# Optimization experiments

Hardware: AMD Instinct MI355X
Metric: run time of the kernel (lower is better)

Reference implementation:

```python
import jax, jax.numpy as jnp
import numpy as np

B, N, HID, E, H = 4, 256, 256, 64, 4
OUT = HID // 2          # 128
D = OUT // H            # 32
AGG = H * (2 * D + 1)   # 260 = concat(mean D, attn_sum 1, max D) per head


def setup_inputs() -> dict:
    key = jax.random.key(0)
    ks = jax.random.split(key, 7)
    s = 0.05
    return {
        "h_x": jax.random.normal(ks[0], (B, N, HID), jnp.float32),
        "h_e": jax.random.normal(ks[1], (B, N, N, E), jnp.float32),
        "h_m": jnp.ones((B, N), jnp.float32),
        "W_Q": jax.random.normal(ks[2], (OUT, HID), jnp.float32) * s,
        "W_K": jax.random.normal(ks[3], (OUT, E), jnp.float32) * s,
        "W_V": jax.random.normal(ks[4], (OUT, E), jnp.float32) * s,
        "W_R": jax.random.normal(ks[5], (OUT, AGG), jnp.float32) * s,
    }


def reference(h_x, h_e, h_m, W_Q, W_K, W_V, W_R):
    # queries from node features: [B,H,N,D]
    h_q = (h_x @ W_Q.T).reshape(B, N, H, D).transpose(0, 2, 1, 3)
    # keys/values from dense pairwise edge features: [B,H,N,N,D]
    h_k = jnp.einsum('bnme,ce->bnmc', h_e, W_K).reshape(B, N, N, H, D).transpose(0, 3, 1, 2, 4)
    h_v = jnp.einsum('bnme,ce->bnmc', h_e, W_V).reshape(B, N, N, H, D).transpose(0, 3, 1, 2, 4)
    # broadcast dot: [B,H,N,N]
    scores = jnp.einsum('bhnd,bhnmd->bhnm', h_q, h_k) / np.float32(np.sqrt(D))
    # per-node mask broadcast as [B,1,N,1] (masks query rows)
    scores = jnp.where(h_m[:, None, :, None] == 0, -jnp.inf, scores)
    # NOTE: original code softmaxes over dim=1 = HEAD axis (faithful)
    attn = jax.nn.softmax(scores, axis=1)                      # [B,H,N,N]
    attn_w = attn[..., None] * h_v                             # [B,H,N,N,D]
    aggr_sum = attn_w.sum(axis=3)                              # [B,H,N,D]
    attn_sum = attn.sum(axis=3, keepdims=True) + 1e-8          # [B,H,N,1]
    aggr_mean = aggr_sum / attn_sum
    aggr_max = attn_w.max(axis=3)                              # [B,H,N,D]
    multi = jnp.concatenate([aggr_mean, attn_sum, aggr_max], axis=-1)  # [B,H,N,2D+1]
    aggr_out = multi.transpose(0, 2, 1, 3).reshape(B, N, AGG)  # [B,N,260]
    return aggr_out @ W_R.T                                    # [B,N,OUT]
```

## Files before the change

kernel.cpp:

```cpp
#include <hip/hip_runtime.h>
#include <hip/hip_bf16.h>

constexpr int Bb   = 4;
constexpr int Nn   = 256;
constexpr int HID  = 256;
constexpr int Ee   = 64;
constexpr int Hh   = 4;
constexpr int OUTc = 128;
constexpr int Dd   = 32;
constexpr int AGG  = 260;
constexpr int REC  = 264;
constexpr int QA_LD = 264;

constexpr size_t WS_WRT   = 0;
constexpr size_t WS_FRAGV = WS_WRT + (size_t)AGG * OUTc;
constexpr size_t WS_FRAGQ = WS_FRAGV + 4096;
constexpr size_t WS_UFRAG = WS_FRAGQ + 16384;

typedef __attribute__((ext_vector_type(8))) short short8;
typedef __attribute__((ext_vector_type(4))) float floatx4;

__device__ __forceinline__ unsigned pk2(float a, float b) {
    union { __hip_bfloat162 h; unsigned u; } cv;
    cv.h = __float22bfloat162_rn(float2{a, b});
    return cv.u;
}

__device__ __forceinline__ short8 pack8(floatx4 f0, floatx4 f1) {
    union { short8 s; unsigned u[4]; } r;
    r.u[0] = pk2(f0[0], f0[1]);
    r.u[1] = pk2(f0[2], f0[3]);
    r.u[2] = pk2(f1[0], f1[1]);
    r.u[3] = pk2(f1[2], f1[3]);
    return r.s;
}

__device__ __forceinline__ void gload16(const float* g, float* l) {
    __builtin_amdgcn_global_load_lds(
        (const __attribute__((address_space(1))) void*)g,
        (__attribute__((address_space(3))) void*)l, 16, 0, 0);
}

__global__ __launch_bounds__(256)
void eama_prep(const float* __restrict__ W_Q, const float* __restrict__ W_V,
               const float* __restrict__ W_R, const float* __restrict__ h_x,
               const float* __restrict__ W_K,
               unsigned short* __restrict__ wfragV, float* __restrict__ W_RT,
               unsigned short* __restrict__ ufrag)
{
    __shared__ __align__(16) unsigned short sA[16 * QA_LD];
    __shared__ __align__(16) float sqL[16][132];
    __shared__ __align__(16) float sU2[16][256];

    const int tid = threadIdx.x;
    const int bid = blockIdx.x;

    if (bid < 4) {
        const int e    = bid * 256 + tid;
        const int lane = e & 63;
        const int ks   = (e >> 6) & 1;
        const int ct   = e >> 7;
        const int ncol = lane & 15, q8 = lane >> 4;
        const float* row = W_V + (ct * 16 + ncol) * Ee;
        const int k0 = ks * 32 + q8 * 8;
        floatx4 f0 = *(const floatx4*)(row + k0);
        floatx4 f1 = *(const floatx4*)(row + k0 + 4);
        *(short8*)(wfragV + (size_t)e * 8) = pack8(f0, f1);
        return;
    }
    if (bid < 134) {
        const int i = (bid - 4) * 256 + tid;
        if (i < AGG * OUTc) {
            const int c = i & 127, j = i >> 7;
            W_RT[j * OUTc + c] = W_R[c * AGG + j];
        }
        return;
    }

    const int b0   = (bid - 134) * 16;
    const int lane = tid & 63;
    const int wv   = tid >> 6;
    const int ncol = lane & 15, q8 = lane >> 4;

    short8 bq[2][8];
    #pragma unroll
    for (int ct = 0; ct < 2; ++ct)
        #pragma unroll
        for (int ks = 0; ks < 8; ++ks) {
            const float* row = W_Q + (size_t)(wv * 32 + ct * 16 + ncol) * HID + ks * 32 + q8 * 8;
            bq[ct][ks] = pack8(*(const floatx4*)row, *(const floatx4*)(row + 4));
        }
    #pragma unroll
    for (int i = 0; i < 2; ++i) {
        const int idx = tid + i * 256;
        const int r = idx >> 5, blk = idx & 31;
        const float* src = h_x + (size_t)(b0 + r) * HID + blk * 8;
        floatx4 f0 = *(const floatx4*)(src);
        floatx4 f1 = *(const floatx4*)(src + 4);
        *(short8*)&sA[r * QA_LD + blk * 8] = pack8(f0, f1);
    }
    __syncthreads();
    floatx4 acc[2] = {(floatx4){0,0,0,0}, (floatx4){0,0,0,0}};
    #pragma unroll
    for (int ks = 0; ks < 8; ++ks) {
        short8 a = *(const short8*)&sA[ncol * QA_LD + ks * 32 + q8 * 8];
        acc[0] = __builtin_amdgcn_mfma_f32_16x16x32_bf16(a, bq[0][ks], acc[0], 0, 0, 0);
        acc[1] = __builtin_amdgcn_mfma_f32_16x16x32_bf16(a, bq[1][ks], acc[1], 0, 0, 0);
    }
    #pragma unroll
    for (int ct = 0; ct < 2; ++ct)
        #pragma unroll
        for (int rr = 0; rr < 4; ++rr)
            sqL[q8 * 4 + rr][wv * 32 + ct * 16 + ncol] = acc[ct][rr];
    __syncthreads();

    {
        const int h = wv, e = lane;
        float a16[16];
        #pragma unroll
        for (int i = 0; i < 16; ++i) a16[i] = 0.f;
        #pragma unroll
        for (int d4 = 0; d4 < 8; ++d4) {
            float wk0 = W_K[(h * Dd + d4 * 4 + 0) * Ee + e];
            float wk1 = W_K[(h * Dd + d4 * 4 + 1) * Ee + e];
            float wk2 = W_K[(h * Dd + d4 * 4 + 2) * Ee + e];
            float wk3 = W_K[(h * Dd + d4 * 4 + 3) * Ee + e];
            #pragma unroll
            for (int b16 = 0; b16 < 16; ++b16) {
                floatx4 qv = *(const floatx4*)&sqL[b16][h * Dd + d4 * 4];
                a16[b16] += (qv[0] * wk0 + qv[1] * wk1) + (qv[2] * wk2 + qv[3] * wk3);
            }
        }
        #pragma unroll
        for (int b16 = 0; b16 < 16; ++b16)
            sU2[b16][h * 64 + e] = a16[b16] * (0.1767766952966369f * 1.4426950408889634f);
    }
    __syncthreads();

    #pragma unroll
    for (int k = 0; k < 8; ++k) {
        const int ei   = tid + k * 256;
        const int b16  = ei >> 7;
        const int rest = ei & 127;
        const int ks   = rest >> 6;
        const int l    = rest & 63;
        const int nc   = l & 15, qq = l >> 4;
        short8 v = {0, 0, 0, 0, 0, 0, 0, 0};
        if (nc < Hh) {
            floatx4 f0 = *(const floatx4*)&sU2[b16][nc * 64 + ks * 32 + qq * 8];
            floatx4 f1 = *(const floatx4*)&sU2[b16][nc * 64 + ks * 32 + qq * 8 + 4];
            v = pack8(f0, f1);
        }
        *(short8*)(ufrag + ((size_t)((b0 + b16) * 2 + ks) * 64 + l) * 8) = v;
    }
}

__global__ __launch_bounds__(256, 2)
void eama_full(const float* __restrict__ h_e, const float* __restrict__ h_m,
               const unsigned short* __restrict__ wfragV,
               const unsigned short* __restrict__ ufrag,
               const float* __restrict__ W_RT, float* __restrict__ out)
{
    __shared__ __align__(16) float sStage[4][2][4][64][4];
    __shared__ __align__(16) float sS[4][16][4];
    __shared__ float sVS[4][OUTc];
    __shared__ float sVM[4][OUTc];
    __shared__ float sAS[4][Hh];
    __shared__ float sAsum[Hh];

    float* sM = &sStage[0][0][0][0][0];
    float (*sAcc)[OUTc] = (float (*)[OUTc])(sM + 384);

    const int tid  = threadIdx.x;
    const int lane = tid & 63;
    const int w    = tid >> 6;
    const int ncol = lane & 15;
    const int q8   = lane >> 4;
    const int bn   = blockIdx.x;
    const float maskv = h_m[bn];

    short8 bfV[8][2];
    #pragma unroll
    for (int ct = 0; ct < 8; ++ct)
        #pragma unroll
        for (int ks = 0; ks < 2; ++ks)
            bfV[ct][ks] = *(const short8*)(wfragV + ((size_t)(ct * 2 + ks) * 64 + lane) * 8);
    short8 bu0 = *(const short8*)(ufrag + ((size_t)(bn * 2 + 0) * 64 + lane) * 8);
    short8 bu1 = *(const short8*)(ufrag + ((size_t)(bn * 2 + 1) * 64 + lane) * 8);
    asm volatile("" ::: "memory");

    const float* heb = h_e + (size_t)bn * Nn * Ee;
    const float* arq = heb + (size_t)(w * 64 + ncol) * Ee + q8 * 8;

    #define STAGE(it_, buf_) do { \
        const float* ar_ = arq + (size_t)(it_) * 16 * Ee; \
        gload16(ar_,      &sStage[w][buf_][0][0][0]); \
        gload16(ar_ + 4,  &sStage[w][buf_][1][0][0]); \
        gload16(ar_ + 32, &sStage[w][buf_][2][0][0]); \
        gload16(ar_ + 36, &sStage[w][buf_][3][0][0]); \
    } while (0)

    STAGE(0, 0);
    STAGE(1, 1);

    float vs[8], vm[8], asumH = 0.f;
    #pragma unroll
    for (int ct = 0; ct < 8; ++ct) { vs[ct] = 0.f; vm[ct] = -3.402823466e38f; }

    #pragma unroll
    for (int it = 0; it < 4; ++it) {
        const int buf = it & 1;
        if (it < 3) asm volatile("s_waitcnt vmcnt(4)" ::: "memory");
        else        asm volatile("s_waitcnt vmcnt(0)" ::: "memory");

        floatx4 c0 = *(const floatx4*)&sStage[w][buf][0][lane][0];
        floatx4 c1 = *(const floatx4*)&sStage[w][buf][1][lane][0];
        floatx4 c2 = *(const floatx4*)&sStage[w][buf][2][lane][0];
        floatx4 c3 = *(const floatx4*)&sStage[w][buf][3][lane][0];
        short8 af0 = pack8(c0, c1);
        short8 af1 = pack8(c2, c3);
        if (it < 2) {
            asm volatile("s_waitcnt lgkmcnt(0)" ::: "memory");
            STAGE(it + 2, buf);
        }

        floatx4 accV[8], accS = (floatx4){0, 0, 0, 0};
        #pragma unroll
        for (int ct = 0; ct < 8; ++ct) accV[ct] = (floatx4){0, 0, 0, 0};
        __builtin_amdgcn_s_setprio(1);
        #pragma unroll
        for (int ct = 0; ct < 8; ++ct) {
            accV[ct] = __builtin_amdgcn_mfma_f32_16x16x32_bf16(af0, bfV[ct][0], accV[ct], 0, 0, 0);
            accV[ct] = __builtin_amdgcn_mfma_f32_16x16x32_bf16(af1, bfV[ct][1], accV[ct], 0, 0, 0);
        }
        accS = __builtin_amdgcn_mfma_f32_16x16x32_bf16(af0, bu0, accS, 0, 0, 0);
        accS = __builtin_amdgcn_mfma_f32_16x16x32_bf16(af1, bu1, accS, 0, 0, 0);
        __builtin_amdgcn_s_setprio(0);

        if (ncol < Hh) {
            #pragma unroll
            for (int r = 0; r < 4; ++r)
                sS[w][q8 * 4 + r][ncol] = (maskv != 0.f) ? accS[r] : -1e30f;
        }
        __builtin_amdgcn_wave_barrier();

        #pragma unroll
        for (int r = 0; r < 4; ++r) {
            floatx4 sc = *(const floatx4*)&sS[w][q8 * 4 + r][0];
            float e0 = __builtin_amdgcn_exp2f(sc[0]), e1 = __builtin_amdgcn_exp2f(sc[1]);
            float e2 = __builtin_amdgcn_exp2f(sc[2]), e3 = __builtin_amdgcn_exp2f(sc[3]);
            float inv = __builtin_amdgcn_rcpf((e0 + e1) + (e2 + e3));
            float a0 = e0 * inv, a1 = e1 * inv, a2 = e2 * inv, a3 = e3 * inv;
            asumH += (ncol & 2) ? ((ncol & 1) ? a3 : a2) : ((ncol & 1) ? a1 : a0);
            float p;
            p = a0 * accV[0][r]; vs[0] += p; vm[0] = fmaxf(vm[0], p);
            p = a0 * accV[1][r]; vs[1] += p; vm[1] = fmaxf(vm[1], p);
            p = a1 * accV[2][r]; vs[2] += p; vm[2] = fmaxf(vm[2], p);
            p = a1 * accV[3][r]; vs[3] += p; vm[3] = fmaxf(vm[3], p);
            p = a2 * accV[4][r]; vs[4] += p; vm[4] = fmaxf(vm[4], p);
            p = a2 * accV[5][r]; vs[5] += p; vm[5] = fmaxf(vm[5], p);
            p = a3 * accV[6][r]; vs[6] += p; vm[6] = fmaxf(vm[6], p);
            p = a3 * accV[7][r]; vs[7] += p; vm[7] = fmaxf(vm[7], p);
        }
        __builtin_amdgcn_wave_barrier();
    }
    #undef STAGE

    #pragma unroll
    for (int ct = 0; ct < 8; ++ct) {
        vs[ct] += __shfl_xor(vs[ct], 16, 64);
        vs[ct] += __shfl_xor(vs[ct], 32, 64);
        vm[ct] = fmaxf(vm[ct], __shfl_xor(vm[ct], 16, 64));
        vm[ct] = fmaxf(vm[ct], __shfl_xor(vm[ct], 32, 64));
    }
    asumH += __shfl_xor(asumH, 16, 64);
    asumH += __shfl_xor(asumH, 32, 64);

    if (lane < 16) {
        #pragma unroll
        for (int ct = 0; ct < 8; ++ct) {
            sVS[w][ct * 16 + lane] = vs[ct];
            sVM[w][ct * 16 + lane] = vm[ct];
        }
    }
    if (lane < Hh) sAS[w][lane] = asumH;
    __syncthreads();
    if (tid < Hh) {
        sAsum[tid] = 1e-8f +
            (sAS[0][tid] + sAS[1][tid]) + (sAS[2][tid] + sAS[3][tid]);
    }
    __syncthreads();
    if (tid < OUTc) {
        float vsum = (sVS[0][tid] + sVS[1][tid]) + (sVS[2][tid] + sVS[3][tid]);
        float vmax = fmaxf(fmaxf(sVM[0][tid], sVM[1][tid]), fmaxf(sVM[2][tid], sVM[3][tid]));
        const int h = tid >> 5, d = tid & 31;
        sM[h * 65 + d]      = vsum / sAsum[h];
        sM[h * 65 + 33 + d] = vmax;
        if (tid < Hh) sM[tid * 65 + 32] = sAsum[tid];
    }
    __syncthreads();
    {
        const int c = tid & 127, part = tid >> 7;
        const int j0 = part * 130;
        float a0 = 0.f, a1 = 0.f, a2 = 0.f, a3 = 0.f;
        #pragma unroll 4
        for (int j = j0; j < j0 + 128; j += 4) {
            a0 = fmaf(sM[j],     W_RT[(j)     * OUTc + c], a0);
            a1 = fmaf(sM[j + 1], W_RT[(j + 1) * OUTc + c], a1);
            a2 = fmaf(sM[j + 2], W_RT[(j + 2) * OUTc + c], a2);
            a3 = fmaf(sM[j + 3], W_RT[(j + 3) * OUTc + c], a3);
        }
        a0 = fmaf(sM[j0 + 128], W_RT[(j0 + 128) * OUTc + c], a0);
        a1 = fmaf(sM[j0 + 129], W_RT[(j0 + 129) * OUTc + c], a1);
        sAcc[part][c] = (a0 + a1) + (a2 + a3);
    }
    __syncthreads();
    if (tid < OUTc)
        out[bn * OUTc + tid] = sAcc[0][tid] + sAcc[1][tid];
}

extern "C" void kernel_launch(void* const* d_in, const int* in_sizes, int n_in,
                              void* d_out, int out_size, void* d_ws, size_t ws_size,
                              hipStream_t stream) {
    const float* h_x = (const float*)d_in[0];
    const float* h_e = (const float*)d_in[1];
    const float* h_m = (const float*)d_in[2];
    const float* W_Q = (const float*)d_in[3];
    const float* W_K = (const float*)d_in[4];
    const float* W_V = (const float*)d_in[5];
    const float* W_R = (const float*)d_in[6];
    float* out = (float*)d_out;

    float* ws            = (float*)d_ws;
    float* W_RT          = ws + WS_WRT;
    unsigned short* wfV  = (unsigned short*)(ws + WS_FRAGV);
    unsigned short* ufr  = (unsigned short*)(ws + WS_UFRAG);

    eama_prep<<<dim3(198), dim3(256), 0, stream>>>(W_Q, W_V, W_R, h_x, W_K, wfV, W_RT, ufr);
    eama_full<<<dim3(Bb * Nn), dim3(256), 0, stream>>>(h_e, h_m, wfV, ufr, W_RT, out);
}
```

Baseline: 125.8 us.

## Move V weight fragments to LDS and prefetch edge tiles into registers

The per-wave register copy of the W_V bf16 fragments is replaced by a block-wide LDS copy that is read each iteration before the MFMAs. The global_load_lds double-buffered staging of h_e is replaced by a register prefetch of the next 16-row tile. Launch bounds go from 2 to 4 blocks per CU. The aim is to cut VGPR pressure and raise occupancy so more waves hide the h_e streaming latency, at the cost of extra LDS reads per MFMA and an added block barrier.

```diff
diff --git a/kernel.cpp b/kernel.cpp
--- a/kernel.cpp
+++ b/kernel.cpp
@@ -33,12 +33,6 @@
     r.u[2] = pk2(f1[0], f1[1]);
     r.u[3] = pk2(f1[2], f1[3]);
     return r.s;
-}
-
-__device__ __forceinline__ void gload16(const float* g, float* l) {
-    __builtin_amdgcn_global_load_lds(
-        (const __attribute__((address_space(1))) void*)g,
-        (__attribute__((address_space(3))) void*)l, 16, 0, 0);
 }
 
 __global__ __launch_bounds__(256)
@@ -155,21 +149,20 @@
     }
 }
 
-__global__ __launch_bounds__(256, 2)
+__global__ __launch_bounds__(256, 4)
 void eama_full(const float* __restrict__ h_e, const float* __restrict__ h_m,
                const unsigned short* __restrict__ wfragV,
                const unsigned short* __restrict__ ufrag,
                const float* __restrict__ W_RT, float* __restrict__ out)
 {
-    __shared__ __align__(16) float sStage[4][2][4][64][4];
+    __shared__ __align__(16) unsigned short sBF[1024 * 8];
     __shared__ __align__(16) float sS[4][16][4];
     __shared__ float sVS[4][OUTc];
     __shared__ float sVM[4][OUTc];
     __shared__ float sAS[4][Hh];
     __shared__ float sAsum[Hh];
-
-    float* sM = &sStage[0][0][0][0][0];
-    float (*sAcc)[OUTc] = (float (*)[OUTc])(sM + 384);
+    __shared__ __align__(16) float sM[REC];
+    __shared__ float sAcc[2][OUTc];
 
     const int tid  = threadIdx.x;
     const int lane = tid & 63;
@@ -179,50 +172,40 @@
     const int bn   = blockIdx.x;
     const float maskv = h_m[bn];
 
-    short8 bfV[8][2];
-    #pragma unroll
-    for (int ct = 0; ct < 8; ++ct)
-        #pragma unroll
-        for (int ks = 0; ks < 2; ++ks)
-            bfV[ct][ks] = *(const short8*)(wfragV + ((size_t)(ct * 2 + ks) * 64 + lane) * 8);
+    #pragma unroll
+    for (int i = 0; i < 4; ++i) {
+        const int e = i * 256 + tid;
+        *(floatx4*)&sBF[(size_t)e * 8] = *(const floatx4*)(wfragV + (size_t)e * 8);
+    }
     short8 bu0 = *(const short8*)(ufrag + ((size_t)(bn * 2 + 0) * 64 + lane) * 8);
     short8 bu1 = *(const short8*)(ufrag + ((size_t)(bn * 2 + 1) * 64 + lane) * 8);
-    asm volatile("" ::: "memory");
+    __syncthreads();
 
     const float* heb = h_e + (size_t)bn * Nn * Ee;
     const float* arq = heb + (size_t)(w * 64 + ncol) * Ee + q8 * 8;
 
-    #define STAGE(it_, buf_) do { \
-        const float* ar_ = arq + (size_t)(it_) * 16 * Ee; \
-        gload16(ar_,      &sStage[w][buf_][0][0][0]); \
-        gload16(ar_ + 4,  &sStage[w][buf_][1][0][0]); \
-        gload16(ar_ + 32, &sStage[w][buf_][2][0][0]); \
-        gload16(ar_ + 36, &sStage[w][buf_][3][0][0]); \
-    } while (0)
-
-    STAGE(0, 0);
-    STAGE(1, 1);
-
     float vs[8], vm[8], asumH = 0.f;
     #pragma unroll
     for (int ct = 0; ct < 8; ++ct) { vs[ct] = 0.f; vm[ct] = -3.402823466e38f; }
 
+    floatx4 p0, p1, p2, p3;
+    p0 = *(const floatx4*)(arq);
+    p1 = *(const floatx4*)(arq + 4);
+    p2 = *(const floatx4*)(arq + 32);
+    p3 = *(const floatx4*)(arq + 36);
+
     #pragma unroll
     for (int it = 0; it < 4; ++it) {
-        const int buf = it & 1;
-        if (it < 3) asm volatile("s_waitcnt vmcnt(4)" ::: "memory");
-        else        asm volatile("s_waitcnt vmcnt(0)" ::: "memory");
-
-        floatx4 c0 = *(const floatx4*)&sStage[w][buf][0][lane][0];
-        floatx4 c1 = *(const floatx4*)&sStage[w][buf][1][lane][0];
-        floatx4 c2 = *(const floatx4*)&sStage[w][buf][2][lane][0];
-        floatx4 c3 = *(const floatx4*)&sStage[w][buf][3][lane][0];
-        short8 af0 = pack8(c0, c1);
-        short8 af1 = pack8(c2, c3);
-        if (it < 2) {
-            asm volatile("s_waitcnt lgkmcnt(0)" ::: "memory");
-            STAGE(it + 2, buf);
-        }
+        floatx4 n0, n1, n2, n3;
+        if (it < 3) {
+            const float* ar = arq + (size_t)(it + 1) * 16 * Ee;
+            n0 = *(const floatx4*)(ar);
+            n1 = *(const floatx4*)(ar + 4);
+            n2 = *(const floatx4*)(ar + 32);
+            n3 = *(const floatx4*)(ar + 36);
+        }
+        short8 af0 = pack8(p0, p1);
+        short8 af1 = pack8(p2, p3);
 
         floatx4 accV[8], accS = (floatx4){0, 0, 0, 0};
         #pragma unroll
@@ -230,8 +213,10 @@
         __builtin_amdgcn_s_setprio(1);
         #pragma unroll
         for (int ct = 0; ct < 8; ++ct) {
-            accV[ct] = __builtin_amdgcn_mfma_f32_16x16x32_bf16(af0, bfV[ct][0], accV[ct], 0, 0, 0);
-            accV[ct] = __builtin_amdgcn_mfma_f32_16x16x32_bf16(af1, bfV[ct][1], accV[ct], 0, 0, 0);
+            short8 f0 = *(const short8*)&sBF[((size_t)(ct * 2 + 0) * 64 + lane) * 8];
+            short8 f1 = *(const short8*)&sBF[((size_t)(ct * 2 + 1) * 64 + lane) * 8];
+            accV[ct] = __builtin_amdgcn_mfma_f32_16x16x32_bf16(af0, f0, accV[ct], 0, 0, 0);
+            accV[ct] = __builtin_amdgcn_mfma_f32_16x16x32_bf16(af1, f1, accV[ct], 0, 0, 0);
         }
         accS = __builtin_amdgcn_mfma_f32_16x16x32_bf16(af0, bu0, accS, 0, 0, 0);
         accS = __builtin_amdgcn_mfma_f32_16x16x32_bf16(af1, bu1, accS, 0, 0, 0);
@@ -263,8 +248,8 @@
             p = a3 * accV[7][r]; vs[7] += p; vm[7] = fmaxf(vm[7], p);
         }
         __builtin_amdgcn_wave_barrier();
-    }
-    #undef STAGE
+        p0 = n0; p1 = n1; p2 = n2; p3 = n3;
+    }
 
     #pragma unroll
     for (int ct = 0; ct < 8; ++ct) {
```

Measured after the change: 158.7 us. 26.1% more time.
